# Performance work log

Measured on AMD Instinct MI355X. Metric: run time of the kernel, lower is better.

Reference implementation:

```python
import jax, jax.numpy as jnp
import numpy as np

DIM = 2048
NUM_HEADS = 16
HEAD_DIM = DIM // NUM_HEADS  # 128
ROPE_BASE = 10000.0


def setup_inputs() -> dict:
    key = jax.random.key(0)
    k1, k2, k3 = jax.random.split(key, 3)
    B, S = 2, 2048
    x = jax.random.normal(k1, (B, S, DIM), dtype=jnp.float32)
    # causal mask: 1 where allowed (k <= q), 0 elsewhere
    mask = jnp.tril(jnp.ones((S, S), dtype=jnp.int32))
    # torch Linear(dim, 3*dim, bias=False): store transposed so y = x @ w
    w_qkv = jax.random.normal(k2, (DIM, 3 * DIM), dtype=jnp.float32) / np.sqrt(DIM)
    w_out = jax.random.normal(k3, (DIM, DIM), dtype=jnp.float32) / np.sqrt(DIM)
    return {"x": x, "w_qkv": w_qkv, "w_out": w_out, "mask": mask}


def _rope_cos_sin(seq_len, dtype):
    inv_freq = 1.0 / (ROPE_BASE ** (jnp.arange(0, HEAD_DIM, 2, dtype=jnp.float32) / HEAD_DIM))
    t = jnp.arange(seq_len, dtype=jnp.float32)
    freqs = t[:, None] * inv_freq[None, :]          # [S, D/2]
    emb = jnp.concatenate([freqs, freqs], axis=-1)  # [S, D]
    return jnp.cos(emb).astype(dtype), jnp.sin(emb).astype(dtype)


def _rotate_half(x):
    x1, x2 = jnp.split(x, 2, axis=-1)
    return jnp.concatenate([-x2, x1], axis=-1)


def reference(x, w_qkv, w_out, mask):
    B, S, _ = x.shape
    H, D = NUM_HEADS, HEAD_DIM
    qkv = x @ w_qkv                                   # [B, S, 3*dim]
    qkv = qkv.reshape(B, S, 3, H, D).transpose(2, 0, 3, 1, 4)  # [3, B, H, S, D]
    q, k, v = qkv[0], qkv[1], qkv[2]
    cos, sin = _rope_cos_sin(S, x.dtype)              # [S, D] broadcast over B,H
    q = q * cos + _rotate_half(q) * sin
    k = k * cos + _rotate_half(k) * sin
    scale = D ** -0.5
    score = jnp.einsum("bhqd,bhkd->bhqk", q, k) * scale
    score = jnp.where(mask == 0, -jnp.inf, score)
    attn = jax.nn.softmax(score, axis=-1)             # dropout = identity (eval)
    out = jnp.einsum("bhqk,bhkd->bhqd", attn, v)
    out = out.transpose(0, 2, 1, 3).reshape(B, S, H * D)
    return out @ w_out
```

## Files before the change

kernel.cpp:

```cpp
#include <hip/hip_runtime.h>

typedef __attribute__((ext_vector_type(8))) __bf16 bf16x8;
typedef __attribute__((ext_vector_type(4))) float f32x4;

__device__ __forceinline__ unsigned short f2bf(float x) {
  union { float f; unsigned int u; } v; v.f = x;
  unsigned int r = v.u + 0x7fffu + ((v.u >> 16) & 1u);
  return (unsigned short)(r >> 16);
}
__device__ __forceinline__ float bf2f(unsigned short x) {
  union { unsigned int u; float f; } v; v.u = ((unsigned int)x) << 16;
  return v.f;
}
__device__ __forceinline__ void g2l16(const void* g, void* l) {
  __builtin_amdgcn_global_load_lds((const __attribute__((address_space(1))) void*)g,
                                   (__attribute__((address_space(3))) void*)l, 16, 0, 0);
}

__global__ __launch_bounds__(256) void prep_k(const float* __restrict__ x,
                                              const float* __restrict__ wq,
                                              const float* __restrict__ wo,
                                              unsigned short* __restrict__ xb,
                                              unsigned short* __restrict__ wqT,
                                              unsigned short* __restrict__ woT) {
  __shared__ unsigned short t[64][65];
  const int b = blockIdx.x;
  if (b < 8192) {
    int i = b * 256 + threadIdx.x;
    float4 v = ((const float4*)x)[i];
    ushort4 o;
    o.x = f2bf(v.x); o.y = f2bf(v.y); o.z = f2bf(v.z); o.w = f2bf(v.w);
    ((ushort4*)xb)[i] = o;
    return;
  }
  const float* in; unsigned short* out; int C, c0, r0;
  const int R = 2048;
  if (b < 11264) { int bb = b - 8192;  in = wq; out = wqT; C = 6144; c0 = (bb % 96) * 64; r0 = (bb / 96) * 64; }
  else           { int bb = b - 11264; in = wo; out = woT; C = 2048; c0 = (bb & 31) * 64; r0 = (bb >> 5) * 64; }
  const int tx = threadIdx.x & 63, tg = threadIdx.x >> 6;
#pragma unroll
  for (int i = 0; i < 16; i++) {
    int r = i * 4 + tg;
    t[r][tx] = f2bf(in[(size_t)(r0 + r) * C + c0 + tx]);
  }
  __syncthreads();
#pragma unroll
  for (int i = 0; i < 16; i++) {
    int c = i * 4 + tg;
    out[(size_t)(c0 + c) * R + r0 + tx] = t[tx][c];
  }
}

template <int EPI>
__global__ __launch_bounds__(256) void gemm_bt_k(const unsigned short* __restrict__ A,
                                                 const unsigned short* __restrict__ BT,
                                                 int K, int N,
                                                 float* __restrict__ outF,
                                                 unsigned short* __restrict__ oq,
                                                 unsigned short* __restrict__ ok,
                                                 unsigned short* __restrict__ ov) {
  __shared__ __align__(16) unsigned short smem[16640];
  unsigned short* lA = smem;
  unsigned short* lB = smem + 8192;
  const int tid = threadIdx.x;
  const int w = tid >> 6, lane = tid & 63;
  const int quad = lane >> 4, l16 = lane & 15;
  const int m0 = blockIdx.y * 128, n0 = blockIdx.x * 128;
  const int wm = (w >> 1) * 64, wn = (w & 1) * 64;
  f32x4 acc[4][4] = {};
  const int srow = tid >> 3;
  const int schunk = (tid & 7) ^ (srow & 7);
  const unsigned short* gA = A + (size_t)(m0 + srow) * K + schunk * 8;
  const unsigned short* gB = BT + (size_t)(n0 + srow) * K + schunk * 8;
  char* ldA = (char*)lA + tid * 16;
  char* ldB = (char*)lB + tid * 16;
  const size_t rskip = (size_t)32 * K;
  for (int k0 = 0; k0 < K; k0 += 64) {
#pragma unroll
    for (int j = 0; j < 4; j++) {
      g2l16(gA + k0 + j * rskip, ldA + j * 4096);
      g2l16(gB + k0 + j * rskip, ldB + j * 4096);
    }
    __syncthreads();
#pragma unroll
    for (int ks = 0; ks < 2; ks++) {
      bf16x8 af[4], bfv[4];
#pragma unroll
      for (int i = 0; i < 4; i++)
        af[i] = *(const bf16x8*)((const char*)lA + (size_t)(wm + i * 16 + l16) * 128 +
                                 ((size_t)((ks * 4 + quad) ^ (l16 & 7)) * 16));
#pragma unroll
      for (int j = 0; j < 4; j++)
        bfv[j] = *(const bf16x8*)((const char*)lB + (size_t)(wn + j * 16 + l16) * 128 +
                                  ((size_t)((ks * 4 + quad) ^ (l16 & 7)) * 16));
#pragma unroll
      for (int i = 0; i < 4; i++)
#pragma unroll
        for (int j = 0; j < 4; j++)
          acc[i][j] = __builtin_amdgcn_mfma_f32_16x16x32_bf16(af[i], bfv[j], acc[i][j], 0, 0, 0);
    }
    __syncthreads();
  }
  if (EPI == 0) {
    const int which = n0 >> 11;
    const int h = (n0 >> 7) & 15;
#pragma unroll
    for (int i = 0; i < 4; i++)
#pragma unroll
      for (int r = 0; r < 4; r++) {
        int row = wm + i * 16 + quad * 4 + r;
#pragma unroll
        for (int j = 0; j < 4; j++)
          smem[row * 130 + wn + j * 16 + l16] = f2bf(acc[i][j][r]);
      }
    __syncthreads();
    const int bi2 = m0 >> 11, s0 = m0 & 2047;
    if (which < 2) {
      unsigned short* dst = (which == 0) ? oq : ok;
      const float scale = (which == 0) ? 0.08838834764831845f : 1.0f;
      const int d = tid & 63, tg = tid >> 6;
      const float fr = exp2f(-(float)d * (13.287712379549449f / 64.0f));
      const size_t hb = ((size_t)(bi2 * 16 + h) * 2048 + s0) * 128;
#pragma unroll
      for (int i = 0; i < 32; i++) {
        int r = i * 4 + tg;
        float a = bf2f(smem[r * 130 + d]);
        float bb = bf2f(smem[r * 130 + 64 + d]);
        float sn, cs;
        __sincosf((float)(s0 + r) * fr, &sn, &cs);
        dst[hb + (size_t)r * 128 + d]      = f2bf((a * cs - bb * sn) * scale);
        dst[hb + (size_t)r * 128 + 64 + d] = f2bf((bb * cs + a * sn) * scale);
      }
    } else {
      const int d = tid >> 1, sh = (tid & 1) * 64;
      const size_t vr = ((size_t)(bi2 * 16 + h) * 128 + d) * 2048 + s0 + sh;
#pragma unroll
      for (int v = 0; v < 8; v++) {
        unsigned short tmp[8];
#pragma unroll
        for (int e = 0; e < 8; e++) tmp[e] = smem[(sh + v * 8 + e) * 130 + d];
        *(uint4*)(ov + vr + v * 8) = *(const uint4*)tmp;
      }
    }
  } else {
#pragma unroll
    for (int i = 0; i < 4; i++)
#pragma unroll
      for (int r = 0; r < 4; r++) {
        size_t rowb = (size_t)(m0 + wm + i * 16 + quad * 4 + r) * N;
#pragma unroll
        for (int j = 0; j < 4; j++)
          outF[rowb + n0 + wn + j * 16 + l16] = acc[i][j][r];
      }
  }
}

__global__ __launch_bounds__(256, 2) void attn_k(const unsigned short* __restrict__ qb,
                                                 const unsigned short* __restrict__ kb,
                                                 const unsigned short* __restrict__ vt,
                                                 unsigned short* __restrict__ ob) {
  __shared__ __align__(16) unsigned short lK[64 * 128];
  __shared__ __align__(16) unsigned short lV[128 * 64];
  __shared__ __align__(16) __bf16 pbuf[4][32 * 72];
  const int tid = threadIdx.x;
  const int w = tid >> 6, lane = tid & 63;
  const int quad = lane >> 4, l16 = lane & 15;
  const int qt = (blockIdx.y < 16) ? (int)blockIdx.x : 15 - (int)blockIdx.x;
  const int bh = blockIdx.y;
  const int bi = bh >> 4, h = bh & 15;
  const int q0w = qt * 128 + w * 32;
  const unsigned short* qp = qb + (size_t)bh * 2048 * 128;
  const unsigned short* kp = kb + (size_t)bh * 2048 * 128;
  const unsigned short* vp = vt + (size_t)bh * 128 * 2048;
  __bf16* pw = pbuf[w];

  bf16x8 qf[2][4];
#pragma unroll
  for (int rg = 0; rg < 2; rg++) {
    const unsigned short* qr = qp + (size_t)(q0w + rg * 16 + l16) * 128 + quad * 8;
#pragma unroll
    for (int st = 0; st < 4; st++) qf[rg][st] = *(const bf16x8*)(qr + st * 32);
  }
  f32x4 o[2][8] = {};
  f32x4 lsum[2] = {};

  const int krow = tid >> 4;
  const int kcg = (tid & 15) ^ krow;
  const int vd = tid >> 3;
  const int vsg = (tid & 7) ^ ((tid >> 3) & 7);
  unsigned short* lKdst = lK + (size_t)tid * 8;
  unsigned short* lVdst = lV + (size_t)tid * 8;

  const int nkt = 2 * qt + 2;
  const int myNkt = (q0w + 31) / 64 + 1;

  uint4 pk[4], pv[4];
#pragma unroll
  for (int j = 0; j < 4; j++) {
    pk[j] = *(const uint4*)(kp + (size_t)(j * 16 + krow) * 128 + kcg * 8);
    pv[j] = *(const uint4*)(vp + (size_t)(j * 32 + vd) * 2048 + vsg * 8);
  }
  for (int kt = 0; kt < nkt; kt++) {
    const int kt0 = kt * 64;
#pragma unroll
    for (int j = 0; j < 4; j++) {
      *(uint4*)(lKdst + j * 2048) = pk[j];
      *(uint4*)(lVdst + j * 2048) = pv[j];
    }
    __syncthreads();
    if (kt + 1 < nkt) {
      const int kn = kt0 + 64;
#pragma unroll
      for (int j = 0; j < 4; j++) {
        pk[j] = *(const uint4*)(kp + (size_t)(kn + j * 16 + krow) * 128 + kcg * 8);
        pv[j] = *(const uint4*)(vp + (size_t)(j * 32 + vd) * 2048 + kn + vsg * 8);
      }
    }
    if (kt < myNkt) {
      f32x4 sc[2][4] = {};
#pragma unroll
      for (int ct = 0; ct < 4; ct++) {
        const int nrow = ct * 16 + l16;
#pragma unroll
        for (int st = 0; st < 4; st++) {
          bf16x8 kf = *(const bf16x8*)(lK + ((size_t)nrow * 16 + ((st * 4 + quad) ^ l16)) * 8);
          sc[0][ct] = __builtin_amdgcn_mfma_f32_16x16x32_bf16(qf[0][st], kf, sc[0][ct], 0, 0, 0);
          sc[1][ct] = __builtin_amdgcn_mfma_f32_16x16x32_bf16(qf[1][st], kf, sc[1][ct], 0, 0, 0);
        }
      }
      const bool needmask = (kt == myNkt - 1);
#pragma unroll
      for (int rg = 0; rg < 2; rg++)
#pragma unroll
        for (int ct = 0; ct < 4; ct++) {
          const int col = kt0 + ct * 16 + l16;
          const int rowb = q0w + rg * 16 + quad * 4;
#pragma unroll
          for (int r = 0; r < 4; r++) {
            float s = sc[rg][ct][r];
            if (needmask && col > rowb + r) s = -1e30f;
            float e = __expf(s);
            lsum[rg][r] += e;
            pw[(rg * 16 + quad * 4 + r) * 72 + ct * 16 + l16] = (__bf16)e;
          }
        }
      bf16x8 pf[2][2];
#pragma unroll
      for (int rg = 0; rg < 2; rg++)
#pragma unroll
        for (int sb = 0; sb < 2; sb++)
          pf[rg][sb] = *(const bf16x8*)(pw + (rg * 16 + l16) * 72 + sb * 32 + quad * 8);
#pragma unroll
      for (int dt = 0; dt < 8; dt++) {
#pragma unroll
        for (int sb = 0; sb < 2; sb++) {
          bf16x8 vf = *(const bf16x8*)(lV +
              ((size_t)(dt * 16 + l16) * 8 + ((sb * 4 + quad) ^ (l16 & 7))) * 8);
          o[0][dt] = __builtin_amdgcn_mfma_f32_16x16x32_bf16(pf[0][sb], vf, o[0][dt], 0, 0, 0);
          o[1][dt] = __builtin_amdgcn_mfma_f32_16x16x32_bf16(pf[1][sb], vf, o[1][dt], 0, 0, 0);
        }
      }
    }
    __syncthreads();
  }
#pragma unroll
  for (int m = 1; m < 16; m <<= 1)
#pragma unroll
    for (int rg = 0; rg < 2; rg++)
#pragma unroll
      for (int r = 0; r < 4; r++)
        lsum[rg][r] += __shfl_xor(lsum[rg][r], m, 64);
  float inv[2][4];
#pragma unroll
  for (int rg = 0; rg < 2; rg++)
#pragma unroll
    for (int r = 0; r < 4; r++) inv[rg][r] = 1.0f / lsum[rg][r];
#pragma unroll
  for (int rg = 0; rg < 2; rg++)
#pragma unroll
    for (int dt = 0; dt < 8; dt++)
#pragma unroll
      for (int r = 0; r < 4; r++)
        ob[(size_t)(bi * 2048 + q0w + rg * 16 + quad * 4 + r) * 2048 + h * 128 + dt * 16 + l16] =
            f2bf(o[rg][dt][r] * inv[rg][r]);
}

extern "C" void kernel_launch(void* const* d_in, const int* in_sizes, int n_in,
                              void* d_out, int out_size, void* d_ws, size_t ws_size,
                              hipStream_t stream) {
  const float* x = (const float*)d_in[0];
  const float* wqkv = (const float*)d_in[1];
  const float* wout = (const float*)d_in[2];
  char* ws = (char*)d_ws;
  const size_t MiB = 1ull << 20;
  unsigned short* xb    = (unsigned short*)(ws + 0);
  unsigned short* wqkvT = (unsigned short*)(ws + 16 * MiB);
  unsigned short* woutT = (unsigned short*)(ws + 40 * MiB);
  unsigned short* qb    = (unsigned short*)(ws + 48 * MiB);
  unsigned short* kb    = (unsigned short*)(ws + 64 * MiB);
  unsigned short* vtb   = (unsigned short*)(ws + 80 * MiB);
  unsigned short* attnb = (unsigned short*)(ws + 96 * MiB);
  float* outF = (float*)d_out;

  prep_k<<<12288, 256, 0, stream>>>(x, wqkv, wout, xb, wqkvT, woutT);
  gemm_bt_k<0><<<dim3(48, 32), 256, 0, stream>>>(xb, wqkvT, 2048, 6144, nullptr, qb, kb, vtb);
  attn_k<<<dim3(16, 32), 256, 0, stream>>>(qb, kb, vtb, attnb);
  gemm_bt_k<1><<<dim3(16, 32), 256, 0, stream>>>(attnb, woutT, 2048, 2048, outF,
                                                 nullptr, nullptr, nullptr);
}
```

Measured before the change: 438.5 us.

## Load attention K/V tiles directly to LDS and vectorize V transpose epilogue

The attention kernel drops its register-staged prefetch of the next K/V tile and instead issues direct global-to-LDS loads for the current tile just before the barrier. This removes register pressure and the LDS write instructions, but it also removes the overlap of next-tile loads with compute, so load latency is exposed each iteration unless other waves hide it. The QKV GEMM epilogue for V now writes accumulators to LDS transposed with 4-element vector stores and a padded stride, then reads 16-byte rows for coalesced global stores. This replaces the scalar gather that built each vector. LDS use grows slightly to fit the padded transpose buffer.

```diff
diff --git a/kernel.cpp b/kernel.cpp
--- a/kernel.cpp
+++ b/kernel.cpp
@@ -59,7 +59,7 @@
                                                  unsigned short* __restrict__ oq,
                                                  unsigned short* __restrict__ ok,
                                                  unsigned short* __restrict__ ov) {
-  __shared__ __align__(16) unsigned short smem[16640];
+  __shared__ __align__(16) unsigned short smem[17408];
   unsigned short* lA = smem;
   unsigned short* lB = smem + 8192;
   const int tid = threadIdx.x;
@@ -104,18 +104,18 @@
   if (EPI == 0) {
     const int which = n0 >> 11;
     const int h = (n0 >> 7) & 15;
-#pragma unroll
-    for (int i = 0; i < 4; i++)
-#pragma unroll
-      for (int r = 0; r < 4; r++) {
-        int row = wm + i * 16 + quad * 4 + r;
-#pragma unroll
-        for (int j = 0; j < 4; j++)
-          smem[row * 130 + wn + j * 16 + l16] = f2bf(acc[i][j][r]);
-      }
-    __syncthreads();
     const int bi2 = m0 >> 11, s0 = m0 & 2047;
     if (which < 2) {
+#pragma unroll
+      for (int i = 0; i < 4; i++)
+#pragma unroll
+        for (int r = 0; r < 4; r++) {
+          int row = wm + i * 16 + quad * 4 + r;
+#pragma unroll
+          for (int j = 0; j < 4; j++)
+            smem[row * 130 + wn + j * 16 + l16] = f2bf(acc[i][j][r]);
+        }
+      __syncthreads();
       unsigned short* dst = (which == 0) ? oq : ok;
       const float scale = (which == 0) ? 0.08838834764831845f : 1.0f;
       const int d = tid & 63, tg = tid >> 6;
@@ -132,14 +132,25 @@
         dst[hb + (size_t)r * 128 + 64 + d] = f2bf((bb * cs + a * sn) * scale);
       }
     } else {
-      const int d = tid >> 1, sh = (tid & 1) * 64;
-      const size_t vr = ((size_t)(bi2 * 16 + h) * 128 + d) * 2048 + s0 + sh;
+#pragma unroll
+      for (int i = 0; i < 4; i++)
+#pragma unroll
+        for (int j = 0; j < 4; j++) {
+          int row = wm + i * 16 + quad * 4;
+          int col = wn + j * 16 + l16;
+          ushort4 t4;
+          t4.x = f2bf(acc[i][j][0]); t4.y = f2bf(acc[i][j][1]);
+          t4.z = f2bf(acc[i][j][2]); t4.w = f2bf(acc[i][j][3]);
+          *(ushort4*)&smem[col * 136 + row] = t4;
+        }
+      __syncthreads();
+      const int sc = tid & 15, dbase = tid >> 4;
+      const size_t vrb = ((size_t)(bi2 * 16 + h) * 128) * 2048 + s0;
 #pragma unroll
       for (int v = 0; v < 8; v++) {
-        unsigned short tmp[8];
-#pragma unroll
-        for (int e = 0; e < 8; e++) tmp[e] = smem[(sh + v * 8 + e) * 130 + d];
-        *(uint4*)(ov + vr + v * 8) = *(const uint4*)tmp;
+        int d = dbase + v * 16;
+        uint4 val = *(const uint4*)&smem[d * 136 + sc * 8];
+        *(uint4*)(ov + vrb + (size_t)d * 2048 + sc * 8) = val;
       }
     }
   } else {
@@ -193,29 +204,14 @@
 
   const int nkt = 2 * qt + 2;
   const int myNkt = (q0w + 31) / 64 + 1;
-
-  uint4 pk[4], pv[4];
-#pragma unroll
-  for (int j = 0; j < 4; j++) {
-    pk[j] = *(const uint4*)(kp + (size_t)(j * 16 + krow) * 128 + kcg * 8);
-    pv[j] = *(const uint4*)(vp + (size_t)(j * 32 + vd) * 2048 + vsg * 8);
-  }
   for (int kt = 0; kt < nkt; kt++) {
     const int kt0 = kt * 64;
 #pragma unroll
     for (int j = 0; j < 4; j++) {
-      *(uint4*)(lKdst + j * 2048) = pk[j];
-      *(uint4*)(lVdst + j * 2048) = pv[j];
+      g2l16(kp + (size_t)(kt0 + j * 16 + krow) * 128 + kcg * 8, lKdst + j * 2048);
+      g2l16(vp + (size_t)(j * 32 + vd) * 2048 + kt0 + vsg * 8, lVdst + j * 2048);
     }
     __syncthreads();
-    if (kt + 1 < nkt) {
-      const int kn = kt0 + 64;
-#pragma unroll
-      for (int j = 0; j < 4; j++) {
-        pk[j] = *(const uint4*)(kp + (size_t)(kn + j * 16 + krow) * 128 + kcg * 8);
-        pv[j] = *(const uint4*)(vp + (size_t)(j * 32 + vd) * 2048 + kn + vsg * 8);
-      }
-    }
     if (kt < myNkt) {
       f32x4 sc[2][4] = {};
 #pragma unroll
```

Result: faster. 377.4 us (-13.9%).
